# Kernel tuning notes

Hardware: AMD Instinct MI355X
Metric: run time of the kernel (lower is better)

The kernel has to match this reference:

```python
import jax, jax.numpy as jnp
import numpy as np
from jax import lax

NUM_CLASSES = 5
NUM_TASKS = 20
CONV_CHANS = [(64, 3), (64, 64), (128, 64), (128, 128), (256, 128), (256, 256)]  # (out, in)


def setup_inputs() -> dict:
    key = jax.random.key(0)
    ks = jax.random.split(key, 16)
    B = 512
    x = jax.random.normal(ks[0], (B, 3, 32, 32), dtype=jnp.float32)
    tid = jax.random.randint(ks[1], (B,), 0, NUM_TASKS)
    inp = {"x": x, "tid": tid}
    for i, (oc, ic) in enumerate(CONV_CHANS):
        fan_in = ic * 9
        inp[f"w{i}"] = jax.random.normal(ks[2 + 2 * i], (oc, ic, 3, 3), dtype=jnp.float32) * np.float32((2.0 / fan_in) ** 0.5)
        inp[f"b{i}"] = jnp.zeros((oc,), dtype=jnp.float32)
    inp["cw"] = jax.random.normal(ks[14], (NUM_CLASSES * NUM_TASKS, 4096), dtype=jnp.float32) * np.float32(4096 ** -0.5)
    inp["cb"] = jnp.zeros((NUM_CLASSES * NUM_TASKS,), dtype=jnp.float32)
    return inp


def _conv_relu(x, w, b):
    y = lax.conv_general_dilated(x, w, window_strides=(1, 1), padding='SAME',
                                 dimension_numbers=('NCHW', 'OIHW', 'NCHW'))
    return jax.nn.relu(y + b[None, :, None, None])


def _maxpool2(x):
    return lax.reduce_window(x, -jnp.inf, lax.max, (1, 1, 2, 2), (1, 1, 2, 2), 'VALID')


def _forward(x, tid, ws, bs, cw, cb):
    # VGG cfg [64,64,'M',128,128,'M',256,256,'M']
    h = _conv_relu(x, ws[0], bs[0])
    h = _conv_relu(h, ws[1], bs[1])
    h = _maxpool2(h)
    h = _conv_relu(h, ws[2], bs[2])
    h = _conv_relu(h, ws[3], bs[3])
    h = _maxpool2(h)
    h = _conv_relu(h, ws[4], bs[4])
    h = _conv_relu(h, ws[5], bs[5])
    h = _maxpool2(h)                      # [B, 256, 4, 4]
    feat = h.reshape(h.shape[0], -1)      # [B, 4096], matches torch NCHW flatten
    # Batched task-indexed classifier: gather each sample's 5-row weight block.
    w_sel = cw.reshape(NUM_TASKS, NUM_CLASSES, 4096)[tid]   # [B, 5, 4096]
    b_sel = cb.reshape(NUM_TASKS, NUM_CLASSES)[tid]         # [B, 5]
    return jnp.einsum('bcd,bd->bc', w_sel, feat) + b_sel


def reference(x, tid, w0, b0, w1, b1, w2, b2, w3, b3, w4, b4, w5, b5, cw, cb):
    ws = (w0, w1, w2, w3, w4, w5)
    bs = (b0, b1, b2, b3, b4, b5)
    return _forward(x, tid, ws, bs, cw, cb)
```

## Files before the change

### kernel.cpp

```cpp
#include <hip/hip_runtime.h>


typedef __attribute__((ext_vector_type(8))) short short8;
typedef __attribute__((ext_vector_type(4))) float floatx4;
typedef unsigned int uint;
typedef unsigned short ushort;

__device__ __forceinline__ ushort f2bf(float f) {
    uint u = __float_as_uint(f);
    return (ushort)((u + 0x7fffu + ((u >> 16) & 1u)) >> 16);
}
__device__ __forceinline__ float bf2f(ushort h) {
    return __uint_as_float(((uint)h) << 16);
}

__global__ __launch_bounds__(256) void wtransform_lin(
    const float* __restrict__ src, short* __restrict__ dst, int OC, int IC)
{
    int n = 9 * OC * IC;
    int o = blockIdx.x * 256 + threadIdx.x;
    if (o >= n) return;
    int j    = o & 7;
    int lane = (o >> 3) & 63;
    int r    = o >> 9;
    int G16  = OC >> 4;
    int g    = r % G16;  r /= G16;
    int kk   = r % 9;
    int icb  = r / 9;
    int oc = g * 16 + (lane & 15);
    int ic = icb * 32 + (lane >> 4) * 8 + j;
    dst[o] = (short)f2bf(src[((long)oc * IC + ic) * 9 + kk]);
}

__global__ __launch_bounds__(256) void wtransform0(
    const float* __restrict__ src, short* __restrict__ dst)
{
    int idx = blockIdx.x * 256 + threadIdx.x;
    if (idx >= 64 * 32) return;
    int oc = idx >> 5, k = idx & 31;
    dst[idx] = (k < 27) ? (short)f2bf(src[oc * 27 + k]) : (short)0;
}

__global__ __launch_bounds__(256, 2) void conv0_mfma(
    const float* __restrict__ x, const short* __restrict__ wT0,
    const float* __restrict__ b0, ushort* __restrict__ out)
{
    __shared__ float  s_x[3 * 18 * 34];
    __shared__ ushort s_b[4 * 512 * 8];

    const int tid  = threadIdx.x;
    const int wv   = tid >> 6;
    const int lane = tid & 63;
    const int quad = lane >> 4;
    const int l16  = lane & 15;
    const int b    = blockIdx.x >> 1;
    const int r0   = (blockIdx.x & 1) * 16;

    for (int idx = tid; idx < 3 * 18 * 34; idx += 256) {
        int c   = idx / 612;
        int rem = idx - c * 612;
        int ry  = rem / 34, rx = rem - ry * 34;
        int gy  = r0 + ry - 1, gx = rx - 1;
        float v = 0.f;
        if (gy >= 0 && gy < 32 && gx >= 0 && gx < 32)
            v = x[(((long)b * 3 + c) * 32 + gy) * 32 + gx];
        s_x[idx] = v;
    }
    __syncthreads();

#pragma unroll
    for (int rep = 0; rep < 2; ++rep) {
        int pxl = rep * 256 + tid;
        int py = pxl >> 5, px = pxl & 31;
        ushort v[32];
#pragma unroll
        for (int c = 0; c < 3; ++c)
#pragma unroll
            for (int ky = 0; ky < 3; ++ky)
#pragma unroll
                for (int kx = 0; kx < 3; ++kx)
                    v[c * 9 + ky * 3 + kx] = f2bf(s_x[c * 612 + (py + ky) * 34 + (px + kx)]);
#pragma unroll
        for (int k = 27; k < 32; ++k) v[k] = 0;
#pragma unroll
        for (int q = 0; q < 4; ++q)
            *(uint4*)(&s_b[(q * 512 + pxl) * 8]) = *(const uint4*)(v + q * 8);
    }
    __syncthreads();

    floatx4 acc[4][8];
#pragma unroll
    for (int i = 0; i < 4; ++i)
#pragma unroll
        for (int t = 0; t < 8; ++t) acc[i][t] = (floatx4)0.f;

    short8 afr[4];
#pragma unroll
    for (int i = 0; i < 4; ++i)
        afr[i] = *(const short8*)(wT0 + (i * 16 + l16) * 32 + quad * 8);
#pragma unroll
    for (int t = 0; t < 8; ++t) {
        int pxl = wv * 128 + t * 16 + l16;
        short8 bfr = *(const short8*)(&s_b[(quad * 512 + pxl) * 8]);
#pragma unroll
        for (int i = 0; i < 4; ++i)
            acc[i][t] = __builtin_amdgcn_mfma_f32_16x16x32_bf16(afr[i], bfr, acc[i][t], 0, 0, 0);
    }

#pragma unroll
    for (int i = 0; i < 4; ++i) {
        int oc0 = i * 16 + quad * 4;
        float4 bv = *(const float4*)(b0 + oc0);
#pragma unroll
        for (int t = 0; t < 8; ++t) {
            int pxl = wv * 128 + t * 16 + l16;
            int py = pxl >> 5, px = pxl & 31;
            long dst = ((((long)b * 8 + (oc0 >> 3)) * 32 + r0 + py) * 32 + px) * 8 + (oc0 & 7);
            float v0 = acc[i][t][0] + bv.x;
            float v1 = acc[i][t][1] + bv.y;
            float v2 = acc[i][t][2] + bv.z;
            float v3 = acc[i][t][3] + bv.w;
            ushort o[4];
            o[0] = f2bf(v0 > 0.f ? v0 : 0.f);
            o[1] = f2bf(v1 > 0.f ? v1 : 0.f);
            o[2] = f2bf(v2 > 0.f ? v2 : 0.f);
            o[3] = f2bf(v3 > 0.f ? v3 : 0.f);
            *(uint2*)(out + dst) = *(uint2*)o;
        }
    }
}

template<int IC, int OC, int H, int W, int ROWS, int OCGROUPS, bool POOL>
__global__ __launch_bounds__(256, 2) void conv_so(
    const ushort* __restrict__ act_in,
    const short*  __restrict__ wTs,
    const float*  __restrict__ bias,
    ushort* __restrict__ act_out)
{
    constexpr int WPAD  = W + 2;
    constexpr int RPAD  = ROWS + 2;
    constexpr int UNITS = RPAD * WPAD;
    constexpr int SEGS  = H / ROWS;
    constexpr int C8I   = IC / 8;
    constexpr int CPUP  = C8I + 1;
    constexpr int G16   = OC / 16;
    constexpr int NICB  = IC / 32;
    constexpr int C8O   = OC / 8;
    constexpr int TMAX  = NICB * 9;

    __shared__ ushort s_act[UNITS * CPUP * 8];

    const int tid  = threadIdx.x;
    const int wv   = tid >> 6;
    const int lane = tid & 63;
    const int quad = lane >> 4;
    const int l16  = lane & 15;

    const int b   = blockIdx.x / SEGS;
    const int seg = blockIdx.x - b * SEGS;
    const int r0  = seg * ROWS;
    const int ocg = wv % OCGROUPS;
    const int pxg = wv / OCGROUPS;

    for (int c = tid; c < UNITS * C8I; c += 256) {
        int sub  = c / UNITS;
        int unit = c - sub * UNITS;
        int ry   = unit / WPAD, cx = unit - ry * WPAD;
        int gy   = r0 + ry - 1, gx = cx - 1;
        uint4 val = make_uint4(0, 0, 0, 0);
        if ((unsigned)gy < (unsigned)H && (unsigned)gx < (unsigned)W) {
            long src = ((((long)b * C8I + sub) * H + gy) * W + gx) * 8;
            val = *(const uint4*)(act_in + src);
        }
        *(uint4*)(&s_act[((size_t)unit * CPUP + sub) * 8]) = val;
    }
    __syncthreads();

    floatx4 acc[4][4];
#pragma unroll
    for (int i = 0; i < 4; ++i)
#pragma unroll
        for (int t = 0; t < 4; ++t) acc[i][t] = (floatx4)0.f;

    int bbase[4];
#pragma unroll
    for (int t = 0; t < 4; ++t) {
        int pxl = pxg * 64 + t * 16 + l16;
        int py  = pxl / W, px = pxl - py * W;
        bbase[t] = (py * WPAD + px) * CPUP * 8;
    }

    const short8* wb = (const short8*)wTs;
    short8 afr[4];
#pragma unroll
    for (int i = 0; i < 4; ++i)
        afr[i] = wb[((long)0 * G16 + ocg * 4 + i) * 64 + lane];

    int tl = 0;
    for (int icb = 0; icb < NICB; ++icb) {
#pragma unroll
        for (int kk = 0; kk < 9; ++kk) {
            const int ky = kk / 3, kx = kk - ky * 3;
            const int koff = ((ky * WPAD + kx) * CPUP + icb * 4 + quad) * 8;
            short8 bfr[4];
#pragma unroll
            for (int t = 0; t < 4; ++t)
                bfr[t] = *(const short8*)(&s_act[bbase[t] + koff]);
            int tn = (tl + 1 < TMAX) ? tl + 1 : tl;
            short8 afrN[4];
#pragma unroll
            for (int i = 0; i < 4; ++i)
                afrN[i] = wb[((long)tn * G16 + ocg * 4 + i) * 64 + lane];
#pragma unroll
            for (int i = 0; i < 4; ++i)
#pragma unroll
                for (int t = 0; t < 4; ++t)
                    acc[i][t] = __builtin_amdgcn_mfma_f32_16x16x32_bf16(
                        afr[i], bfr[t], acc[i][t], 0, 0, 0);
#pragma unroll
            for (int i = 0; i < 4; ++i) afr[i] = afrN[i];
            ++tl;
        }
    }

    if constexpr (!POOL) {
#pragma unroll
        for (int i = 0; i < 4; ++i) {
            int oc0 = ocg * 64 + i * 16 + quad * 4;
            float4 bv = *(const float4*)(bias + oc0);
#pragma unroll
            for (int t = 0; t < 4; ++t) {
                int pxl = pxg * 64 + t * 16 + l16;
                int py  = pxl / W, px = pxl - py * W;
                long dst = ((((long)b * C8O + (oc0 >> 3)) * H + r0 + py) * W + px) * 8 + (oc0 & 7);
                float v0 = acc[i][t][0] + bv.x;
                float v1 = acc[i][t][1] + bv.y;
                float v2 = acc[i][t][2] + bv.z;
                float v3 = acc[i][t][3] + bv.w;
                ushort o[4];
                o[0] = f2bf(v0 > 0.f ? v0 : 0.f);
                o[1] = f2bf(v1 > 0.f ? v1 : 0.f);
                o[2] = f2bf(v2 > 0.f ? v2 : 0.f);
                o[3] = f2bf(v3 > 0.f ? v3 : 0.f);
                *(uint2*)(act_out + dst) = *(uint2*)o;
            }
        }
    } else {
        __syncthreads();
        ushort* s_pool = s_act;
        constexpr int PSTR = OC + 8;
        static_assert(ROWS * W * PSTR <= UNITS * CPUP * 8, "pool scratch fits");
#pragma unroll
        for (int i = 0; i < 4; ++i) {
            int oc0 = ocg * 64 + i * 16 + quad * 4;
            float4 bv = *(const float4*)(bias + oc0);
#pragma unroll
            for (int t = 0; t < 4; ++t) {
                int pxl = pxg * 64 + t * 16 + l16;
                float v0 = acc[i][t][0] + bv.x;
                float v1 = acc[i][t][1] + bv.y;
                float v2 = acc[i][t][2] + bv.z;
                float v3 = acc[i][t][3] + bv.w;
                ushort o[4];
                o[0] = f2bf(v0 > 0.f ? v0 : 0.f);
                o[1] = f2bf(v1 > 0.f ? v1 : 0.f);
                o[2] = f2bf(v2 > 0.f ? v2 : 0.f);
                o[3] = f2bf(v3 > 0.f ? v3 : 0.f);
                *(uint2*)(&s_pool[pxl * PSTR + oc0]) = *(uint2*)o;
            }
        }
        __syncthreads();
        constexpr int PH = ROWS / 2, PW = W / 2, HOT = H / 2;
        const int pr0 = r0 / 2;
        for (int u = tid; u < PH * PW * C8O; u += 256) {
            int c8 = u % C8O;
            int pp = u / C8O;
            int xo = pp % PW, yo = pp / PW;
            const ushort* p00 = &s_pool[((2 * yo) * W + 2 * xo) * PSTR + c8 * 8];
            uint4 q0 = *(const uint4*)(p00);
            uint4 q1 = *(const uint4*)(p00 + PSTR);
            uint4 q2 = *(const uint4*)(p00 + W * PSTR);
            uint4 q3 = *(const uint4*)(p00 + W * PSTR + PSTR);
            const ushort* a0 = (const ushort*)&q0;
            const ushort* a1 = (const ushort*)&q1;
            const ushort* a2 = (const ushort*)&q2;
            const ushort* a3 = (const ushort*)&q3;
            ushort r[8];
#pragma unroll
            for (int j = 0; j < 8; ++j) {
                ushort m0 = a0[j] > a1[j] ? a0[j] : a1[j];
                ushort m1 = a2[j] > a3[j] ? a2[j] : a3[j];
                r[j] = m0 > m1 ? m0 : m1;
            }
            long dst = ((((long)b * C8O + c8) * HOT + pr0 + yo) * PW + xo) * 8;
            *(uint4*)(act_out + dst) = *(uint4*)r;
        }
    }
}

__global__ __launch_bounds__(256) void classifier_k(
    const ushort* __restrict__ feat, const int* __restrict__ tids,
    const float* __restrict__ cw, const float* __restrict__ cb,
    float* __restrict__ out, int B)
{
    int g = blockIdx.x * 256 + threadIdx.x;
    int wid = g >> 6, lane = g & 63;
    if (wid >= B * 5) return;
    int b = wid / 5, c = wid - b * 5;
    int t = tids[b];
    const float* wrow = cw + (long)(t * 5 + c) * 4096;
    const ushort* f = feat + (long)b * 4096;
    float s = 0.f;
#pragma unroll 4
    for (int d = lane; d < 4096; d += 64) {
        int fidx = (((d >> 7) * 16) + (d & 15)) * 8 + ((d >> 4) & 7);
        s += wrow[d] * bf2f(f[fidx]);
    }
#pragma unroll
    for (int off = 32; off > 0; off >>= 1) s += __shfl_down(s, off, 64);
    if (lane == 0) out[wid] = s + cb[t * 5 + c];
}

extern "C" void kernel_launch(void* const* d_in, const int* in_sizes, int n_in,
                              void* d_out, int out_size, void* d_ws, size_t ws_size,
                              hipStream_t stream)
{
    const float* x   = (const float*)d_in[0];
    const int*   tid = (const int*)d_in[1];
    const float* w0 = (const float*)d_in[2];  const float* b0 = (const float*)d_in[3];
    const float* w1 = (const float*)d_in[4];  const float* b1 = (const float*)d_in[5];
    const float* w2 = (const float*)d_in[6];  const float* b2 = (const float*)d_in[7];
    const float* w3 = (const float*)d_in[8];  const float* b3 = (const float*)d_in[9];
    const float* w4 = (const float*)d_in[10]; const float* b4 = (const float*)d_in[11];
    const float* w5 = (const float*)d_in[12]; const float* b5 = (const float*)d_in[13];
    const float* cw = (const float*)d_in[14];
    const float* cb = (const float*)d_in[15];
    float* outp = (float*)d_out;

    const int B = in_sizes[0] / (3 * 32 * 32);

    short* wt0  = (short*)d_ws;
    short* wts1 = wt0 + 2048;
    short* wts2 = wts1 + 36864;
    short* wts3 = wts2 + 73728;
    short* wts4 = wts3 + 147456;
    short* wts5 = wts4 + 294912;
    const size_t WT_HW = 2048 + 36864 + 73728 + 147456 + 294912 + 589824;
    const size_t fixed_bytes = WT_HW * 2;

    int Bc = B;
    while (Bc > 2 && fixed_bytes + (size_t)Bc * 2 * 65536 * 2 > ws_size) Bc >>= 1;
    if (Bc < 2) Bc = 2;

    ushort* bufA = (ushort*)((short*)d_ws + WT_HW);
    ushort* bufB = bufA + (size_t)Bc * 65536;

    wtransform0<<<(64 * 32 + 255) / 256, 256, 0, stream>>>(w0, wt0);
    wtransform_lin<<<(9 * 64 * 64 + 255) / 256, 256, 0, stream>>>(w1, wts1, 64, 64);
    wtransform_lin<<<(9 * 128 * 64 + 255) / 256, 256, 0, stream>>>(w2, wts2, 128, 64);
    wtransform_lin<<<(9 * 128 * 128 + 255) / 256, 256, 0, stream>>>(w3, wts3, 128, 128);
    wtransform_lin<<<(9 * 256 * 128 + 255) / 256, 256, 0, stream>>>(w4, wts4, 256, 128);
    wtransform_lin<<<(9 * 256 * 256 + 255) / 256, 256, 0, stream>>>(w5, wts5, 256, 256);

    for (int cb0 = 0; cb0 < B; cb0 += Bc) {
        const float* xc = x + (size_t)cb0 * 3 * 32 * 32;
        const int* tidc = tid + cb0;
        float* outc = outp + (size_t)cb0 * 5;

        conv0_mfma<<<Bc * 2, 256, 0, stream>>>(xc, wt0, b0, bufA);
        conv_so<64, 64, 32, 32, 8, 1, true><<<Bc * 4, 256, 0, stream>>>(bufA, wts1, b1, bufB);
        conv_so<64, 128, 16, 16, 8, 2, false><<<Bc * 2, 256, 0, stream>>>(bufB, wts2, b2, bufA);
        conv_so<128, 128, 16, 16, 8, 2, true><<<Bc * 2, 256, 0, stream>>>(bufA, wts3, b3, bufB);
        conv_so<128, 256, 8, 8, 8, 4, false><<<Bc, 256, 0, stream>>>(bufB, wts4, b4, bufA);
        conv_so<256, 256, 8, 8, 8, 4, true><<<Bc, 256, 0, stream>>>(bufA, wts5, b5, bufB);
        classifier_k<<<(Bc * 5 * 64 + 255) / 256, 256, 0, stream>>>(bufB, tidc, cw, cb, outc, Bc);
    }
}
```

Before: 314.2 us.

## Stage conv input channels through LDS, split OC across blocks, raise occupancy

Result: slower. 322.4 us (+2.6%).

```diff
diff --git a/kernel.cpp b/kernel.cpp
--- a/kernel.cpp
+++ b/kernel.cpp
@@ -14,12 +14,9 @@
     return __uint_as_float(((uint)h) << 16);
 }
 
-__global__ __launch_bounds__(256) void wtransform_lin(
-    const float* __restrict__ src, short* __restrict__ dst, int OC, int IC)
-{
-    int n = 9 * OC * IC;
-    int o = blockIdx.x * 256 + threadIdx.x;
-    if (o >= n) return;
+__device__ __forceinline__ void wt_lin_one(
+    const float* __restrict__ src, short* __restrict__ dst, int OC, int IC, int o)
+{
     int j    = o & 7;
     int lane = (o >> 3) & 63;
     int r    = o >> 9;
@@ -32,13 +29,29 @@
     dst[o] = (short)f2bf(src[((long)oc * IC + ic) * 9 + kk]);
 }
 
-__global__ __launch_bounds__(256) void wtransform0(
-    const float* __restrict__ src, short* __restrict__ dst)
-{
-    int idx = blockIdx.x * 256 + threadIdx.x;
-    if (idx >= 64 * 32) return;
-    int oc = idx >> 5, k = idx & 31;
-    dst[idx] = (k < 27) ? (short)f2bf(src[oc * 27 + k]) : (short)0;
+__global__ __launch_bounds__(256) void wtransform_all(
+    const float* __restrict__ w0, const float* __restrict__ w1,
+    const float* __restrict__ w2, const float* __restrict__ w3,
+    const float* __restrict__ w4, const float* __restrict__ w5,
+    short* __restrict__ dst0, short* __restrict__ dst1, short* __restrict__ dst2,
+    short* __restrict__ dst3, short* __restrict__ dst4, short* __restrict__ dst5)
+{
+    int o = blockIdx.x * 256 + threadIdx.x;
+    if (o < 2048) {
+        int oc = o >> 5, k = o & 31;
+        dst0[o] = (k < 27) ? (short)f2bf(w0[oc * 27 + k]) : (short)0;
+        return;
+    }
+    o -= 2048;
+    if (o < 36864)  { wt_lin_one(w1, dst1,  64,  64, o); return; }
+    o -= 36864;
+    if (o < 73728)  { wt_lin_one(w2, dst2, 128,  64, o); return; }
+    o -= 73728;
+    if (o < 147456) { wt_lin_one(w3, dst3, 128, 128, o); return; }
+    o -= 147456;
+    if (o < 294912) { wt_lin_one(w4, dst4, 256, 128, o); return; }
+    o -= 294912;
+    if (o < 589824) { wt_lin_one(w5, dst5, 256, 256, o); return; }
 }
 
 __global__ __launch_bounds__(256, 2) void conv0_mfma(
@@ -130,25 +143,34 @@
     }
 }
 
-template<int IC, int OC, int H, int W, int ROWS, int OCGROUPS, bool POOL>
-__global__ __launch_bounds__(256, 2) void conv_so(
+template<int IC, int OC, int H, int W, int ROWS, int OCGROUPS, int OCSPLIT,
+         int NSTAGE, bool POOL>
+__global__ __launch_bounds__(256, 4) void conv_so(
     const ushort* __restrict__ act_in,
     const short*  __restrict__ wTs,
     const float*  __restrict__ bias,
     ushort* __restrict__ act_out)
 {
+    constexpr int PXG   = 4 / OCGROUPS;
+    constexpr int NFRAG = (ROWS * W) / (PXG * 16);
+    constexpr int OCBLK = OCGROUPS * 64;
     constexpr int WPAD  = W + 2;
     constexpr int RPAD  = ROWS + 2;
     constexpr int UNITS = RPAD * WPAD;
     constexpr int SEGS  = H / ROWS;
     constexpr int C8I   = IC / 8;
-    constexpr int CPUP  = C8I + 1;
+    constexpr int C8H   = C8I / NSTAGE;
+    constexpr int CPUP  = C8H + 1;
     constexpr int G16   = OC / 16;
-    constexpr int NICB  = IC / 32;
+    constexpr int NICBH = (IC / 32) / NSTAGE;
     constexpr int C8O   = OC / 8;
-    constexpr int TMAX  = NICB * 9;
-
-    __shared__ ushort s_act[UNITS * CPUP * 8];
+    constexpr int TMAX  = (IC / 32) * 9;
+    constexpr int PSTR  = OCBLK + 8;
+    constexpr int SHW   = UNITS * CPUP * 8;
+    constexpr int PHW   = POOL ? ROWS * W * PSTR : 0;
+    constexpr int LDSHW = SHW > PHW ? SHW : PHW;
+
+    __shared__ ushort s_act[LDSHW];
 
     const int tid  = threadIdx.x;
     const int wv   = tid >> 6;
@@ -156,36 +178,25 @@
     const int quad = lane >> 4;
     const int l16  = lane & 15;
 
-    const int b   = blockIdx.x / SEGS;
-    const int seg = blockIdx.x - b * SEGS;
+    int bx = blockIdx.x;
+    const int ocb = bx % OCSPLIT;  bx /= OCSPLIT;
+    const int seg = bx % SEGS;
+    const int b   = bx / SEGS;
     const int r0  = seg * ROWS;
     const int ocg = wv % OCGROUPS;
     const int pxg = wv / OCGROUPS;
-
-    for (int c = tid; c < UNITS * C8I; c += 256) {
-        int sub  = c / UNITS;
-        int unit = c - sub * UNITS;
-        int ry   = unit / WPAD, cx = unit - ry * WPAD;
-        int gy   = r0 + ry - 1, gx = cx - 1;
-        uint4 val = make_uint4(0, 0, 0, 0);
-        if ((unsigned)gy < (unsigned)H && (unsigned)gx < (unsigned)W) {
-            long src = ((((long)b * C8I + sub) * H + gy) * W + gx) * 8;
-            val = *(const uint4*)(act_in + src);
-        }
-        *(uint4*)(&s_act[((size_t)unit * CPUP + sub) * 8]) = val;
-    }
-    __syncthreads();
-
-    floatx4 acc[4][4];
+    const int gbase = ocb * OCGROUPS * 4 + ocg * 4;
+
+    floatx4 acc[4][NFRAG];
 #pragma unroll
     for (int i = 0; i < 4; ++i)
 #pragma unroll
-        for (int t = 0; t < 4; ++t) acc[i][t] = (floatx4)0.f;
-
-    int bbase[4];
-#pragma unroll
-    for (int t = 0; t < 4; ++t) {
-        int pxl = pxg * 64 + t * 16 + l16;
+        for (int t = 0; t < NFRAG; ++t) acc[i][t] = (floatx4)0.f;
+
+    int bbase[NFRAG];
+#pragma unroll
+    for (int t = 0; t < NFRAG; ++t) {
+        int pxl = pxg * (NFRAG * 16) + t * 16 + l16;
         int py  = pxl / W, px = pxl - py * W;
         bbase[t] = (py * WPAD + px) * CPUP * 8;
     }
@@ -194,43 +205,60 @@
     short8 afr[4];
 #pragma unroll
     for (int i = 0; i < 4; ++i)
-        afr[i] = wb[((long)0 * G16 + ocg * 4 + i) * 64 + lane];
+        afr[i] = wb[((long)0 * G16 + gbase + i) * 64 + lane];
 
     int tl = 0;
-    for (int icb = 0; icb < NICB; ++icb) {
-#pragma unroll
-        for (int kk = 0; kk < 9; ++kk) {
-            const int ky = kk / 3, kx = kk - ky * 3;
-            const int koff = ((ky * WPAD + kx) * CPUP + icb * 4 + quad) * 8;
-            short8 bfr[4];
-#pragma unroll
-            for (int t = 0; t < 4; ++t)
-                bfr[t] = *(const short8*)(&s_act[bbase[t] + koff]);
-            int tn = (tl + 1 < TMAX) ? tl + 1 : tl;
-            short8 afrN[4];
-#pragma unroll
-            for (int i = 0; i < 4; ++i)
-                afrN[i] = wb[((long)tn * G16 + ocg * 4 + i) * 64 + lane];
-#pragma unroll
-            for (int i = 0; i < 4; ++i)
-#pragma unroll
-                for (int t = 0; t < 4; ++t)
-                    acc[i][t] = __builtin_amdgcn_mfma_f32_16x16x32_bf16(
-                        afr[i], bfr[t], acc[i][t], 0, 0, 0);
-#pragma unroll
-            for (int i = 0; i < 4; ++i) afr[i] = afrN[i];
-            ++tl;
+    for (int st = 0; st < NSTAGE; ++st) {
+        if (st) __syncthreads();
+        for (int c = tid; c < UNITS * C8H; c += 256) {
+            int sub  = c / UNITS;
+            int unit = c - sub * UNITS;
+            int ry   = unit / WPAD, cx = unit - ry * WPAD;
+            int gy   = r0 + ry - 1, gx = cx - 1;
+            uint4 val = make_uint4(0, 0, 0, 0);
+            if ((unsigned)gy < (unsigned)H && (unsigned)gx < (unsigned)W) {
+                long src = ((((long)b * C8I + st * C8H + sub) * H + gy) * W + gx) * 8;
+                val = *(const uint4*)(act_in + src);
+            }
+            *(uint4*)(&s_act[((size_t)unit * CPUP + sub) * 8]) = val;
+        }
+        __syncthreads();
+
+        for (int icb = 0; icb < NICBH; ++icb) {
+#pragma unroll
+            for (int kk = 0; kk < 9; ++kk) {
+                const int ky = kk / 3, kx = kk - ky * 3;
+                const int koff = ((ky * WPAD + kx) * CPUP + icb * 4 + quad) * 8;
+                short8 bfr[NFRAG];
+#pragma unroll
+                for (int t = 0; t < NFRAG; ++t)
+                    bfr[t] = *(const short8*)(&s_act[bbase[t] + koff]);
+                int tn = (tl + 1 < TMAX) ? tl + 1 : tl;
+                short8 afrN[4];
+#pragma unroll
+                for (int i = 0; i < 4; ++i)
+                    afrN[i] = wb[((long)tn * G16 + gbase + i) * 64 + lane];
+#pragma unroll
+                for (int i = 0; i < 4; ++i)
+#pragma unroll
+                    for (int t = 0; t < NFRAG; ++t)
+                        acc[i][t] = __builtin_amdgcn_mfma_f32_16x16x32_bf16(
+                            afr[i], bfr[t], acc[i][t], 0, 0, 0);
+#pragma unroll
+                for (int i = 0; i < 4; ++i) afr[i] = afrN[i];
+                ++tl;
+            }
         }
     }
 
     if constexpr (!POOL) {
 #pragma unroll
         for (int i = 0; i < 4; ++i) {
-            int oc0 = ocg * 64 + i * 16 + quad * 4;
+            int oc0 = ocb * OCBLK + ocg * 64 + i * 16 + quad * 4;
             float4 bv = *(const float4*)(bias + oc0);
 #pragma unroll
-            for (int t = 0; t < 4; ++t) {
-                int pxl = pxg * 64 + t * 16 + l16;
+            for (int t = 0; t < NFRAG; ++t) {
+                int pxl = pxg * (NFRAG * 16) + t * 16 + l16;
                 int py  = pxl / W, px = pxl - py * W;
                 long dst = ((((long)b * C8O + (oc0 >> 3)) * H + r0 + py) * W + px) * 8 + (oc0 & 7);
                 float v0 = acc[i][t][0] + bv.x;
@@ -248,15 +276,13 @@
     } else {
         __syncthreads();
         ushort* s_pool = s_act;
-        constexpr int PSTR = OC + 8;
-        static_assert(ROWS * W * PSTR <= UNITS * CPUP * 8, "pool scratch fits");
 #pragma unroll
         for (int i = 0; i < 4; ++i) {
-            int oc0 = ocg * 64 + i * 16 + quad * 4;
-            float4 bv = *(const float4*)(bias + oc0);
-#pragma unroll
-            for (int t = 0; t < 4; ++t) {
-                int pxl = pxg * 64 + t * 16 + l16;
+            int ocl = ocg * 64 + i * 16 + quad * 4;
+            float4 bv = *(const float4*)(bias + ocb * OCBLK + ocl);
+#pragma unroll
+            for (int t = 0; t < NFRAG; ++t) {
+                int pxl = pxg * (NFRAG * 16) + t * 16 + l16;
                 float v0 = acc[i][t][0] + bv.x;
                 float v1 = acc[i][t][1] + bv.y;
                 float v2 = acc[i][t][2] + bv.z;
@@ -266,15 +292,15 @@
                 o[1] = f2bf(v1 > 0.f ? v1 : 0.f);
                 o[2] = f2bf(v2 > 0.f ? v2 : 0.f);
                 o[3] = f2bf(v3 > 0.f ? v3 : 0.f);
-                *(uint2*)(&s_pool[pxl * PSTR + oc0]) = *(uint2*)o;
+                *(uint2*)(&s_pool[pxl * PSTR + ocl]) = *(uint2*)o;
             }
         }
         __syncthreads();
-        constexpr int PH = ROWS / 2, PW = W / 2, HOT = H / 2;
+        constexpr int PH = ROWS / 2, PW = W / 2, HOT = H / 2, C8B = OCBLK / 8;
         const int pr0 = r0 / 2;
-        for (int u = tid; u < PH * PW * C8O; u += 256) {
-            int c8 = u % C8O;
-            int pp = u / C8O;
+        for (int u = tid; u < PH * PW * C8B; u += 256) {
+            int c8 = u % C8B;
+            int pp = u / C8B;
             int xo = pp % PW, yo = pp / PW;
             const ushort* p00 = &s_pool[((2 * yo) * W + 2 * xo) * PSTR + c8 * 8];
             uint4 q0 = *(const uint4*)(p00);
@@ -292,7 +318,7 @@
                 ushort m1 = a2[j] > a3[j] ? a2[j] : a3[j];
                 r[j] = m0 > m1 ? m0 : m1;
             }
-            long dst = ((((long)b * C8O + c8) * HOT + pr0 + yo) * PW + xo) * 8;
+            long dst = ((((long)b * C8O + ocb * C8B + c8) * HOT + pr0 + yo) * PW + xo) * 8;
             *(uint4*)(act_out + dst) = *(uint4*)r;
         }
     }
@@ -355,12 +381,8 @@
     ushort* bufA = (ushort*)((short*)d_ws + WT_HW);
     ushort* bufB = bufA + (size_t)Bc * 65536;
 
-    wtransform0<<<(64 * 32 + 255) / 256, 256, 0, stream>>>(w0, wt0);
-    wtransform_lin<<<(9 * 64 * 64 + 255) / 256, 256, 0, stream>>>(w1, wts1, 64, 64);
-    wtransform_lin<<<(9 * 128 * 64 + 255) / 256, 256, 0, stream>>>(w2, wts2, 128, 64);
-    wtransform_lin<<<(9 * 128 * 128 + 255) / 256, 256, 0, stream>>>(w3, wts3, 128, 128);
-    wtransform_lin<<<(9 * 256 * 128 + 255) / 256, 256, 0, stream>>>(w4, wts4, 256, 128);
-    wtransform_lin<<<(9 * 256 * 256 + 255) / 256, 256, 0, stream>>>(w5, wts5, 256, 256);
+    wtransform_all<<<(int)((WT_HW + 255) / 256), 256, 0, stream>>>(
+        w0, w1, w2, w3, w4, w5, wt0, wts1, wts2, wts3, wts4, wts5);
 
     for (int cb0 = 0; cb0 < B; cb0 += Bc) {
         const float* xc = x + (size_t)cb0 * 3 * 32 * 32;
@@ -368,11 +390,11 @@
         float* outc = outp + (size_t)cb0 * 5;
 
         conv0_mfma<<<Bc * 2, 256, 0, stream>>>(xc, wt0, b0, bufA);
-        conv_so<64, 64, 32, 32, 8, 1, true><<<Bc * 4, 256, 0, stream>>>(bufA, wts1, b1, bufB);
-        conv_so<64, 128, 16, 16, 8, 2, false><<<Bc * 2, 256, 0, stream>>>(bufB, wts2, b2, bufA);
-        conv_so<128, 128, 16, 16, 8, 2, true><<<Bc * 2, 256, 0, stream>>>(bufA, wts3, b3, bufB);
-        conv_so<128, 256, 8, 8, 8, 4, false><<<Bc, 256, 0, stream>>>(bufB, wts4, b4, bufA);
-        conv_so<256, 256, 8, 8, 8, 4, true><<<Bc, 256, 0, stream>>>(bufA, wts5, b5, bufB);
+        conv_so<64, 64, 32, 32, 8, 1, 1, 2, true><<<Bc * 4, 256, 0, stream>>>(bufA, wts1, b1, bufB);
+        conv_so<64, 128, 16, 16, 8, 2, 1, 1, false><<<Bc * 2, 256, 0, stream>>>(bufB, wts2, b2, bufA);
+        conv_so<128, 128, 16, 16, 8, 2, 1, 2, true><<<Bc * 2, 256, 0, stream>>>(bufA, wts3, b3, bufB);
+        conv_so<128, 256, 8, 8, 8, 2, 2, 1, false><<<Bc * 2, 256, 0, stream>>>(bufB, wts4, b4, bufA);
+        conv_so<256, 256, 8, 8, 8, 2, 2, 2, true><<<Bc * 2, 256, 0, stream>>>(bufA, wts5, b5, bufB);
         classifier_k<<<(Bc * 5 * 64 + 255) / 256, 256, 0, stream>>>(bufB, tidc, cw, cb, outc, Bc);
     }
 }
```
